# Optimization experiments

Hardware: AMD Instinct MI355X
Metric: run time of the kernel (lower is better)

The kernel has to match this reference:

```python
import jax, jax.numpy as jnp
import numpy as np

MIN_VARIANCE = 0.1
W_MEAN = 1.0
W_DIST = 1.0
W_DISP = 1.0


def setup_inputs() -> dict:
    key = jax.random.key(0)
    k1, k2 = jax.random.split(key)
    cluster1 = jax.random.normal(k1, (8192, 128), dtype=jnp.float32)
    cluster2 = jax.random.normal(k2, (8192, 128), dtype=jnp.float32)
    return {"cluster1": cluster1, "cluster2": cluster2}


def _mean_loss(c1, c2):
    m1 = jnp.mean(c1, axis=0)
    m2 = jnp.mean(c2, axis=0)
    return jnp.mean((m1 - m2) ** 2)  # F.mse_loss default 'mean'


def _distance_loss(c1, c2):
    # min_j ||c1_i - c2_j||^2, fused via ||a||^2 - 2 a b^T + ||b||^2
    sq1 = jnp.sum(c1 * c1, axis=1)  # [N1]
    sq2 = jnp.sum(c2 * c2, axis=1)  # [N2]
    cross = c1 @ c2.T               # [N1, N2]
    d2 = sq1[:, None] - 2.0 * cross + sq2[None, :]
    return jnp.mean(jnp.min(d2, axis=1))


def _dispersion_loss(c, min_variance=MIN_VARIANCE):
    mean = jnp.mean(c, axis=0)
    variances = jnp.mean((c - mean) ** 2, axis=0)
    return jnp.mean(jax.nn.relu(min_variance - variances))


def reference(cluster1, cluster2):
    return (W_MEAN * _mean_loss(cluster1, cluster2)
            + W_DIST * _distance_loss(cluster1, cluster2)
            + W_DISP * _dispersion_loss(cluster1))
```

## Files before the change

kernel.cpp:

```cpp
#include <hip/hip_runtime.h>
#include <hip/hip_bf16.h>

#define N_ROWS 8192
#define DIMS   128

typedef __bf16 bf16x8 __attribute__((ext_vector_type(8)));
typedef float  f32x4  __attribute__((ext_vector_type(4)));

struct alignas(8) B4 { __hip_bfloat16 h0, h1, h2, h3; };

template <int CTRL>
__device__ __forceinline__ float fmin_dpp(float v) {
    int o = __builtin_amdgcn_update_dpp(0, __float_as_int(v), CTRL, 0xF, 0xF, true);
    return fminf(v, __int_as_float(o));
}

__global__ __launch_bounds__(256) void prep_k(const float* __restrict__ c1,
                                              const float* __restrict__ c2,
                                              __hip_bfloat16* __restrict__ c1b,
                                              __hip_bfloat16* __restrict__ c2b,
                                              float* __restrict__ sq1,
                                              float* __restrict__ sq2,
                                              float* __restrict__ part) {
    const int tid  = threadIdx.x;
    const int lane = tid & 63;
    const int wave = tid >> 6;
    const int half = lane >> 5;
    const int l32  = lane & 31;
    const int cl   = blockIdx.x >> 7;
    const int blk  = blockIdx.x & 127;

    const float* __restrict__ src    = cl ? c2 : c1;
    __hip_bfloat16* __restrict__ dst = cl ? c2b : c1b;
    float* __restrict__ sq           = cl ? sq2 : sq1;
    const float scale                = cl ? 1.0f : -2.0f;

    float4 cs = {0.f, 0.f, 0.f, 0.f};
    float4 cq = {0.f, 0.f, 0.f, 0.f};

    #pragma unroll 4
    for (int i = 0; i < 8; ++i) {
        const int row = blk * 64 + wave * 16 + i * 2 + half;
        float4 x = *reinterpret_cast<const float4*>(src + (size_t)row * DIMS + l32 * 4);
        B4 b4{__float2bfloat16(scale * x.x), __float2bfloat16(scale * x.y),
              __float2bfloat16(scale * x.z), __float2bfloat16(scale * x.w)};
        const int eoff = cl ? (l32 * 4) : ((l32 * 4) ^ ((row & 7) << 3));
        *reinterpret_cast<B4*>(dst + (size_t)row * DIMS + eoff) = b4;
        float s = x.x * x.x + x.y * x.y + x.z * x.z + x.w * x.w;
        #pragma unroll
        for (int m = 16; m; m >>= 1) s += __shfl_xor(s, m);
        if (l32 == 0) sq[row] = s;
        cs.x += x.x; cs.y += x.y; cs.z += x.z; cs.w += x.w;
        cq.x += x.x * x.x; cq.y += x.y * x.y; cq.z += x.z * x.z; cq.w += x.w * x.w;
    }

    cs.x += __shfl_xor(cs.x, 32); cs.y += __shfl_xor(cs.y, 32);
    cs.z += __shfl_xor(cs.z, 32); cs.w += __shfl_xor(cs.w, 32);
    cq.x += __shfl_xor(cq.x, 32); cq.y += __shfl_xor(cq.y, 32);
    cq.z += __shfl_xor(cq.z, 32); cq.w += __shfl_xor(cq.w, 32);

    __shared__ float4 lds4[4][32];
    lds4[wave][l32] = cs;
    __syncthreads();
    if (tid < 32) {
        float4 a = lds4[0][tid], b = lds4[1][tid], c = lds4[2][tid], d = lds4[3][tid];
        float4 t = {a.x + b.x + c.x + d.x, a.y + b.y + c.y + d.y,
                    a.z + b.z + c.z + d.z, a.w + b.w + c.w + d.w};
        const int base = cl ? 32768 : 0;
        part[base + (4 * tid + 0) * 128 + blk] = t.x;
        part[base + (4 * tid + 1) * 128 + blk] = t.y;
        part[base + (4 * tid + 2) * 128 + blk] = t.z;
        part[base + (4 * tid + 3) * 128 + blk] = t.w;
    }
    __syncthreads();
    lds4[wave][l32] = cq;
    __syncthreads();
    if (tid < 32 && cl == 0) {
        float4 a = lds4[0][tid], b = lds4[1][tid], c = lds4[2][tid], d = lds4[3][tid];
        float4 t = {a.x + b.x + c.x + d.x, a.y + b.y + c.y + d.y,
                    a.z + b.z + c.z + d.z, a.w + b.w + c.w + d.w};
        part[16384 + (4 * tid + 0) * 128 + blk] = t.x;
        part[16384 + (4 * tid + 1) * 128 + blk] = t.y;
        part[16384 + (4 * tid + 2) * 128 + blk] = t.z;
        part[16384 + (4 * tid + 3) * 128 + blk] = t.w;
    }
}

__global__ __attribute__((amdgpu_flat_work_group_size(256, 256),
                          amdgpu_waves_per_eu(2, 2)))
void dist_k(const __hip_bfloat16* __restrict__ c1bs,
            const __hip_bfloat16* __restrict__ c2b,
            const float* __restrict__ sq2,
            float* __restrict__ pmin) {
    __shared__ uint4 smem4[4096];
    char* smem = (char*)smem4;

    const int tid  = threadIdx.x;
    const int lane = tid & 63;
    const int wv   = tid >> 6;
    const int lo = lane & 15;
    const int hi = lane >> 4;

    const int b  = blockIdx.x;
    const int wg = (b & 7) * 128 + (b >> 3);
    const int rg = wg >> 5;
    const int cb = wg & 31;
    const int row0 = rg * 256;
    const int col0 = cb * 256 + wv * 64;

    {
        const char* gsrc = (const char*)c1bs + (size_t)row0 * 256;
        #pragma unroll
        for (int i = 0; i < 16; ++i) {
            const int off = i * 4096 + wv * 1024;
            __builtin_amdgcn_global_load_lds(
                (const __attribute__((address_space(1))) unsigned int*)
                    (const void*)(gsrc + off + lane * 16),
                (__attribute__((address_space(3))) unsigned int*)
                    (void*)(smem + off),
                16, 0, 0);
        }
    }

    uint4 b_u[4][4];
    float sq2t[4];
    #pragma unroll
    for (int ct = 0; ct < 4; ++ct) {
        const int J = col0 + ct * 16 + lo;
        sq2t[ct] = sq2[J];
        #pragma unroll
        for (int ks = 0; ks < 4; ++ks)
            b_u[ct][ks] = *reinterpret_cast<const uint4*>(
                c2b + (size_t)J * DIMS + ks * 32 + hi * 8);
    }

    #pragma unroll
    for (int ct = 0; ct < 4; ++ct)
        #pragma unroll
        for (int ks = 0; ks < 4; ++ks)
            asm volatile("" : "+v"(b_u[ct][ks].x), "+v"(b_u[ct][ks].y),
                              "+v"(b_u[ct][ks].z), "+v"(b_u[ct][ks].w));

    asm volatile("s_waitcnt vmcnt(0)" ::: "memory");
    __syncthreads();

    const int swz = (lo & 7) << 4;
    for (int rt = 0; rt < 16; ++rt) {
        bf16x8 a[4];
        #pragma unroll
        for (int ks = 0; ks < 4; ++ks) {
            const int boff = (rt * 16 + lo) * 256 + ((ks * 64 + hi * 16) ^ swz);
            a[ks] = *reinterpret_cast<const bf16x8*>(smem + boff);
        }

        float mrow[4] = {__builtin_inff(), __builtin_inff(),
                         __builtin_inff(), __builtin_inff()};

        __builtin_amdgcn_s_setprio(1);
        #pragma unroll
        for (int ct = 0; ct < 4; ++ct) {
            f32x4 acc = {sq2t[ct], sq2t[ct], sq2t[ct], sq2t[ct]};
            #pragma unroll
            for (int ks = 0; ks < 4; ++ks)
                acc = __builtin_amdgcn_mfma_f32_16x16x32_bf16(
                    a[ks], __builtin_bit_cast(bf16x8, b_u[ct][ks]), acc, 0, 0, 0);
            #pragma unroll
            for (int r = 0; r < 4; ++r)
                mrow[r] = fminf(mrow[r], acc[r]);
        }
        __builtin_amdgcn_s_setprio(0);

        #pragma unroll
        for (int r = 0; r < 4; ++r) {
            float v = mrow[r];
            v = fmin_dpp<0xB1>(v);
            v = fmin_dpp<0x4E>(v);
            v = fmin_dpp<0x141>(v);
            v = fmin_dpp<0x140>(v);
            mrow[r] = v;
        }
        if (lo == 0) {
            #pragma unroll
            for (int r = 0; r < 4; ++r) {
                const int row = row0 + rt * 16 + hi * 4 + r;
                pmin[(size_t)row * 128 + cb * 4 + wv] = mrow[r];
            }
        }
    }
}

__global__ __launch_bounds__(256) void reduce_k(const float* __restrict__ pmin,
                                                const float* __restrict__ sq1,
                                                float* __restrict__ rpart) {
    __shared__ float red[256];
    const int tid = threadIdx.x;
    const int row = blockIdx.x * 256 + tid;

    const float4* p = reinterpret_cast<const float4*>(pmin + (size_t)row * 128);
    float4 m4 = p[0];
    #pragma unroll
    for (int i = 1; i < 32; ++i) {
        float4 v = p[i];
        m4.x = fminf(m4.x, v.x); m4.y = fminf(m4.y, v.y);
        m4.z = fminf(m4.z, v.z); m4.w = fminf(m4.w, v.w);
    }
    float m = fminf(fminf(m4.x, m4.y), fminf(m4.z, m4.w)) + sq1[row];

    red[tid] = m;
    __syncthreads();
    for (int off = 128; off; off >>= 1) {
        if (tid < off) red[tid] += red[tid + off];
        __syncthreads();
    }
    if (tid == 0) rpart[blockIdx.x] = red[0];
}

__global__ __launch_bounds__(256) void final_k(const float* __restrict__ rpart,
                                               const float* __restrict__ part,
                                               float* __restrict__ out) {
    __shared__ float red[256];
    __shared__ float cs[384];
    const int tid = threadIdx.x;

    for (int j = tid; j < 384; j += 256) {
        const float4* p = reinterpret_cast<const float4*>(part + j * 128);
        float4 a = {0.f, 0.f, 0.f, 0.f};
        #pragma unroll 8
        for (int b = 0; b < 32; ++b) {
            float4 v = p[b];
            a.x += v.x; a.y += v.y; a.z += v.z; a.w += v.w;
        }
        cs[j] = a.x + a.y + a.z + a.w;
    }

    float s = (tid < 32) ? rpart[tid] : 0.0f;

    __syncthreads();
    float m = 0.f;
    if (tid < DIMS) {
        const float inv_n = 1.0f / N_ROWS;
        float m1 = cs[tid] * inv_n;
        float vq = cs[128 + tid] * inv_n;
        float m2 = cs[256 + tid] * inv_n;
        float d  = m1 - m2;
        float var = vq - m1 * m1;
        m = d * d + fmaxf(0.1f - var, 0.0f);
    }

    red[tid] = s * (1.0f / N_ROWS) + m * (1.0f / DIMS);
    __syncthreads();
    for (int off = 128; off; off >>= 1) {
        if (tid < off) red[tid] += red[tid + off];
        __syncthreads();
    }
    if (tid == 0) out[0] = red[0];
}

extern "C" void kernel_launch(void* const* d_in, const int* in_sizes, int n_in,
                              void* d_out, int out_size, void* d_ws, size_t ws_size,
                              hipStream_t stream) {
    (void)in_sizes; (void)n_in; (void)out_size; (void)ws_size;
    const float* c1 = (const float*)d_in[0];
    const float* c2 = (const float*)d_in[1];

    char* ws = (char*)d_ws;
    __hip_bfloat16* c1b = (__hip_bfloat16*)ws;
    __hip_bfloat16* c2b = (__hip_bfloat16*)(ws + (1u << 21));
    float* sq1          = (float*)(ws + (1u << 22));
    float* sq2          = sq1 + N_ROWS;
    float* pmin         = sq2 + N_ROWS;
    float* part         = pmin + (size_t)N_ROWS * 128;
    float* rpart        = part + 3 * 16384;

    prep_k<<<256, 256, 0, stream>>>(c1, c2, c1b, c2b, sq1, sq2, part);
    dist_k<<<1024, 256, 0, stream>>>(c1b, c2b, sq2, pmin);
    reduce_k<<<32, 256, 0, stream>>>(pmin, sq1, rpart);
    final_k<<<1, 256, 0, stream>>>(rpart, part, (float*)d_out);
}
```

Before: 51.25 us.

## Halve distance grid with two column blocks per workgroup; fuse reduce and final kernels

The distance kernel now launches 512 workgroups instead of 1024. Each workgroup loads its 256-row A tile into LDS once and loops over two 256-column B blocks, so LDS staging of A is amortised. The separate reduce and final kernels are merged into one tail kernel that uses an atomic counter to pick a last block for the final reduction, removing one launch. The cost is that the XCD-aware block remapping is gone, B loads are serialized per column block, and occupancy is halved across the GPU.

```diff
diff --git a/kernel.cpp b/kernel.cpp
--- a/kernel.cpp
+++ b/kernel.cpp
@@ -21,7 +21,8 @@
                                               __hip_bfloat16* __restrict__ c2b,
                                               float* __restrict__ sq1,
                                               float* __restrict__ sq2,
-                                              float* __restrict__ part) {
+                                              float* __restrict__ part,
+                                              int* __restrict__ cnt) {
     const int tid  = threadIdx.x;
     const int lane = tid & 63;
     const int wave = tid >> 6;
@@ -29,6 +30,8 @@
     const int l32  = lane & 31;
     const int cl   = blockIdx.x >> 7;
     const int blk  = blockIdx.x & 127;
+
+    if (blockIdx.x == 0 && tid == 0) *cnt = 0;
 
     const float* __restrict__ src    = cl ? c2 : c1;
     __hip_bfloat16* __restrict__ dst = cl ? c2b : c1b;
@@ -100,13 +103,9 @@
     const int wv   = tid >> 6;
     const int lo = lane & 15;
     const int hi = lane >> 4;
-
-    const int b  = blockIdx.x;
-    const int wg = (b & 7) * 128 + (b >> 3);
-    const int rg = wg >> 5;
-    const int cb = wg & 31;
+    const int rg = blockIdx.x >> 4;
+    const int cp = blockIdx.x & 15;
     const int row0 = rg * 256;
-    const int col0 = cb * 256 + wv * 64;
 
     {
         const char* gsrc = (const char*)c1bs + (size_t)row0 * 256;
@@ -121,81 +120,92 @@
                 16, 0, 0);
         }
     }
-
-    uint4 b_u[4][4];
-    float sq2t[4];
-    #pragma unroll
-    for (int ct = 0; ct < 4; ++ct) {
-        const int J = col0 + ct * 16 + lo;
-        sq2t[ct] = sq2[J];
-        #pragma unroll
-        for (int ks = 0; ks < 4; ++ks)
-            b_u[ct][ks] = *reinterpret_cast<const uint4*>(
-                c2b + (size_t)J * DIMS + ks * 32 + hi * 8);
-    }
-
-    #pragma unroll
-    for (int ct = 0; ct < 4; ++ct)
-        #pragma unroll
-        for (int ks = 0; ks < 4; ++ks)
-            asm volatile("" : "+v"(b_u[ct][ks].x), "+v"(b_u[ct][ks].y),
-                              "+v"(b_u[ct][ks].z), "+v"(b_u[ct][ks].w));
-
     asm volatile("s_waitcnt vmcnt(0)" ::: "memory");
     __syncthreads();
 
     const int swz = (lo & 7) << 4;
-    for (int rt = 0; rt < 16; ++rt) {
-        bf16x8 a[4];
-        #pragma unroll
-        for (int ks = 0; ks < 4; ++ks) {
-            const int boff = (rt * 16 + lo) * 256 + ((ks * 64 + hi * 16) ^ swz);
-            a[ks] = *reinterpret_cast<const bf16x8*>(smem + boff);
-        }
-
-        float mrow[4] = {__builtin_inff(), __builtin_inff(),
-                         __builtin_inff(), __builtin_inff()};
-
-        __builtin_amdgcn_s_setprio(1);
+
+    #pragma unroll 1
+    for (int c = 0; c < 2; ++c) {
+        const int cb = cp * 2 + c;
+        const int col0 = cb * 256 + wv * 64;
+
+        uint4 b_u[4][4];
+        float sq2t[4];
         #pragma unroll
         for (int ct = 0; ct < 4; ++ct) {
-            f32x4 acc = {sq2t[ct], sq2t[ct], sq2t[ct], sq2t[ct]};
+            const int J = col0 + ct * 16 + lo;
+            sq2t[ct] = sq2[J];
             #pragma unroll
             for (int ks = 0; ks < 4; ++ks)
-                acc = __builtin_amdgcn_mfma_f32_16x16x32_bf16(
-                    a[ks], __builtin_bit_cast(bf16x8, b_u[ct][ks]), acc, 0, 0, 0);
-            #pragma unroll
-            for (int r = 0; r < 4; ++r)
-                mrow[r] = fminf(mrow[r], acc[r]);
-        }
-        __builtin_amdgcn_s_setprio(0);
-
-        #pragma unroll
-        for (int r = 0; r < 4; ++r) {
-            float v = mrow[r];
-            v = fmin_dpp<0xB1>(v);
-            v = fmin_dpp<0x4E>(v);
-            v = fmin_dpp<0x141>(v);
-            v = fmin_dpp<0x140>(v);
-            mrow[r] = v;
-        }
-        if (lo == 0) {
+                b_u[ct][ks] = *reinterpret_cast<const uint4*>(
+                    c2b + (size_t)J * DIMS + ks * 32 + hi * 8);
+        }
+        #pragma unroll
+        for (int ct = 0; ct < 4; ++ct)
+            #pragma unroll
+            for (int ks = 0; ks < 4; ++ks)
+                asm volatile("" : "+v"(b_u[ct][ks].x), "+v"(b_u[ct][ks].y),
+                                  "+v"(b_u[ct][ks].z), "+v"(b_u[ct][ks].w));
+
+        for (int rt = 0; rt < 16; ++rt) {
+            bf16x8 a[4];
+            #pragma unroll
+            for (int ks = 0; ks < 4; ++ks) {
+                const int boff = (rt * 16 + lo) * 256 + ((ks * 64 + hi * 16) ^ swz);
+                a[ks] = *reinterpret_cast<const bf16x8*>(smem + boff);
+            }
+
+            float mrow[4] = {__builtin_inff(), __builtin_inff(),
+                             __builtin_inff(), __builtin_inff()};
+
+            __builtin_amdgcn_s_setprio(1);
+            #pragma unroll
+            for (int ct = 0; ct < 4; ++ct) {
+                f32x4 acc = {sq2t[ct], sq2t[ct], sq2t[ct], sq2t[ct]};
+                #pragma unroll
+                for (int ks = 0; ks < 4; ++ks)
+                    acc = __builtin_amdgcn_mfma_f32_16x16x32_bf16(
+                        a[ks], __builtin_bit_cast(bf16x8, b_u[ct][ks]), acc, 0, 0, 0);
+                #pragma unroll
+                for (int r = 0; r < 4; ++r)
+                    mrow[r] = fminf(mrow[r], acc[r]);
+            }
+            __builtin_amdgcn_s_setprio(0);
+
             #pragma unroll
             for (int r = 0; r < 4; ++r) {
-                const int row = row0 + rt * 16 + hi * 4 + r;
-                pmin[(size_t)row * 128 + cb * 4 + wv] = mrow[r];
-            }
-        }
-    }
-}
-
-__global__ __launch_bounds__(256) void reduce_k(const float* __restrict__ pmin,
-                                                const float* __restrict__ sq1,
-                                                float* __restrict__ rpart) {
+                float v = mrow[r];
+                v = fmin_dpp<0xB1>(v);
+                v = fmin_dpp<0x4E>(v);
+                v = fmin_dpp<0x141>(v);
+                v = fmin_dpp<0x140>(v);
+                mrow[r] = v;
+            }
+            if (lo == 0) {
+                #pragma unroll
+                for (int r = 0; r < 4; ++r) {
+                    const int row = row0 + rt * 16 + hi * 4 + r;
+                    pmin[(size_t)row * 128 + cb * 4 + wv] = mrow[r];
+                }
+            }
+        }
+    }
+}
+
+__global__ __launch_bounds__(256) void tail_k(const float* __restrict__ pmin,
+                                              const float* __restrict__ sq1,
+                                              const float* __restrict__ part,
+                                              float* __restrict__ rscratch,
+                                              float* __restrict__ cscratch,
+                                              int* __restrict__ cnt,
+                                              float* __restrict__ out) {
     __shared__ float red[256];
+    __shared__ int is_last;
+    const int b   = blockIdx.x;
     const int tid = threadIdx.x;
-    const int row = blockIdx.x * 256 + tid;
-
+
+    const int row = b * 256 + tid;
     const float4* p = reinterpret_cast<const float4*>(pmin + (size_t)row * 128);
     float4 m4 = p[0];
     #pragma unroll
@@ -212,42 +222,47 @@
         if (tid < off) red[tid] += red[tid + off];
         __syncthreads();
     }
-    if (tid == 0) rpart[blockIdx.x] = red[0];
-}
-
-__global__ __launch_bounds__(256) void final_k(const float* __restrict__ rpart,
-                                               const float* __restrict__ part,
-                                               float* __restrict__ out) {
-    __shared__ float red[256];
-    __shared__ float cs[384];
-    const int tid = threadIdx.x;
-
-    for (int j = tid; j < 384; j += 256) {
-        const float4* p = reinterpret_cast<const float4*>(part + j * 128);
+    if (tid == 0) rscratch[b] = red[0];
+
+    if (tid < 12) {
+        const int j = b * 12 + tid;
+        const float4* q = reinterpret_cast<const float4*>(part + j * 128);
         float4 a = {0.f, 0.f, 0.f, 0.f};
         #pragma unroll 8
-        for (int b = 0; b < 32; ++b) {
-            float4 v = p[b];
+        for (int k = 0; k < 32; ++k) {
+            float4 v = q[k];
             a.x += v.x; a.y += v.y; a.z += v.z; a.w += v.w;
         }
-        cs[j] = a.x + a.y + a.z + a.w;
-    }
-
-    float s = (tid < 32) ? rpart[tid] : 0.0f;
-
-    __syncthreads();
-    float m = 0.f;
+        cscratch[j] = a.x + a.y + a.z + a.w;
+    }
+
+    __threadfence();
+    __syncthreads();
+    if (tid == 0) {
+        int old = atomicAdd(cnt, 1);
+        is_last = (old == 31) ? 1 : 0;
+    }
+    __syncthreads();
+    if (!is_last) return;
+    __threadfence();
+
+    float s = (tid < 32) ? atomicAdd(&rscratch[tid], 0.0f) : 0.0f;
+
+    float mm = 0.f;
     if (tid < DIMS) {
+        float cs1 = atomicAdd(&cscratch[tid], 0.0f);
+        float cq1 = atomicAdd(&cscratch[128 + tid], 0.0f);
+        float cs2 = atomicAdd(&cscratch[256 + tid], 0.0f);
         const float inv_n = 1.0f / N_ROWS;
-        float m1 = cs[tid] * inv_n;
-        float vq = cs[128 + tid] * inv_n;
-        float m2 = cs[256 + tid] * inv_n;
+        float m1 = cs1 * inv_n;
+        float m2 = cs2 * inv_n;
         float d  = m1 - m2;
-        float var = vq - m1 * m1;
-        m = d * d + fmaxf(0.1f - var, 0.0f);
-    }
-
-    red[tid] = s * (1.0f / N_ROWS) + m * (1.0f / DIMS);
+        float var = cq1 * inv_n - m1 * m1;
+        mm = d * d + fmaxf(0.1f - var, 0.0f);
+    }
+
+    __syncthreads();
+    red[tid] = s * (1.0f / N_ROWS) + mm * (1.0f / DIMS);
     __syncthreads();
     for (int off = 128; off; off >>= 1) {
         if (tid < off) red[tid] += red[tid + off];
@@ -270,10 +285,12 @@
     float* sq2          = sq1 + N_ROWS;
     float* pmin         = sq2 + N_ROWS;
     float* part         = pmin + (size_t)N_ROWS * 128;
-    float* rpart        = part + 3 * 16384;
-
-    prep_k<<<256, 256, 0, stream>>>(c1, c2, c1b, c2b, sq1, sq2, part);
-    dist_k<<<1024, 256, 0, stream>>>(c1b, c2b, sq2, pmin);
-    reduce_k<<<32, 256, 0, stream>>>(pmin, sq1, rpart);
-    final_k<<<1, 256, 0, stream>>>(rpart, part, (float*)d_out);
-}
+    float* rscratch     = part + 3 * 16384;
+    float* cscratch     = rscratch + 32;
+    int*   cnt          = (int*)(cscratch + 384);
+
+    prep_k<<<256, 256, 0, stream>>>(c1, c2, c1b, c2b, sq1, sq2, part, cnt);
+    dist_k<<<512, 256, 0, stream>>>(c1b, c2b, sq2, pmin);
+    tail_k<<<32, 256, 0, stream>>>(pmin, sq1, part, rscratch, cscratch, cnt,
+                                   (float*)d_out);
+}
```

Result: faster. 48.60 us (-5.2%).
